# Optimization experiments

Measured on AMD Instinct MI355X. Metric: run time of the kernel, lower is better.

The kernel has to match this reference:

```python
import jax, jax.numpy as jnp
import numpy as np

N = 50000; E = 800000; G = 64; IN_DIM = 16; HID = 128; VOCAB = 10000; OUT = 768
# (prev_dim, heads, channels_per_head, concat) per GAT layer
LAYERS = [(128, 4, 128, True), (512, 4, 128, True), (512, 1, 128, False)]

def setup_inputs():
    keys = iter(jax.random.split(jax.random.key(0), 80))
    def nrm(shape, s=0.05):
        return jax.random.normal(next(keys), shape, jnp.float32) * s
    inp = {}
    inp["x"] = jax.random.normal(next(keys), (N, IN_DIM), jnp.float32)
    inp["node_ids"] = jax.random.randint(next(keys), (N,), 0, VOCAB)
    inp["edge_index"] = jax.random.randint(next(keys), (2, E), 0, N)
    inp["batch"] = jnp.sort(jax.random.randint(next(keys), (N,), 0, G))
    inp["emb"] = nrm((VOCAB, HID))
    inp["in_W"] = nrm((IN_DIM, HID)); inp["in_b"] = nrm((HID,))
    for i, (p, h, c, cat) in enumerate(LAYERS):
        od = h * c if cat else c
        inp[f"l{i}_lin_W"] = nrm((p, h * c))
        inp[f"l{i}_att_src"] = nrm((h, c))
        inp[f"l{i}_att_dst"] = nrm((h, c))
        inp[f"l{i}_bias"] = nrm((od,))
        inp[f"l{i}_bn_g"] = jnp.ones((od,), jnp.float32)
        inp[f"l{i}_bn_b"] = jnp.zeros((od,), jnp.float32)
        inp[f"l{i}_bn_m"] = nrm((od,))
        inp[f"l{i}_bn_v"] = jax.random.uniform(next(keys), (od,), jnp.float32, 0.5, 1.5)
        inp[f"l{i}_res_W"] = nrm((p, od)); inp[f"l{i}_res_b"] = nrm((od,))
    inp["out_W"] = nrm((2 * 128, OUT)); inp["out_b"] = nrm((OUT,))
    inp["ln_g"] = jnp.ones((OUT,), jnp.float32); inp["ln_b"] = jnp.zeros((OUT,), jnp.float32)
    return inp

def _gat(x, W, a_s, a_d, b, src, dst, h, c, cat):
    # PyG GATConv (eval): lin -> per-edge leaky_relu attention -> segment softmax over dst -> scatter-sum
    n = x.shape[0]
    xl = (x @ W).reshape(n, h, c)                       # [N,H,C]
    e = (xl * a_s).sum(-1)[src] + (xl * a_d).sum(-1)[dst]  # [E,H]
    e = jnp.where(e > 0, e, 0.2 * e)                    # leaky_relu, slope 0.2
    m = jax.ops.segment_max(e, dst, num_segments=n)
    ex = jnp.exp(e - m[dst])
    alpha = ex / jax.ops.segment_sum(ex, dst, num_segments=n)[dst]
    out = jax.ops.segment_sum(xl[src] * alpha[:, :, None], dst, num_segments=n)  # [N,H,C]
    out = out.reshape(n, h * c) if cat else out.mean(axis=1)
    return out + b

def _forward(x, node_ids, edge_index, batch, emb, in_W, in_b, layer_ps, out_W, out_b, ln_g, ln_b):
    n = x.shape[0]
    loop = jnp.arange(n)
    src = jnp.concatenate([edge_index[0], loop])        # GATConv adds self-loops
    dst = jnp.concatenate([edge_index[1], loop])
    h = x @ in_W + in_b + emb[node_ids]
    for (lin_W, a_s, a_d, bias, bn_g, bn_b, bn_m, bn_v, res_W, res_b), (p, nh, c, cat) in zip(layer_ps, LAYERS):
        y = _gat(h, lin_W, a_s, a_d, bias, src, dst, nh, c, cat)
        y = (y - bn_m) / jnp.sqrt(bn_v + 1e-5) * bn_g + bn_b   # BatchNorm1d eval
        y = jax.nn.relu(y)
        h = (h @ res_W + res_b) + y
    cnt = jax.ops.segment_sum(jnp.ones((n,), h.dtype), batch, num_segments=G)
    mean_pool = jax.ops.segment_sum(h, batch, num_segments=G) / jnp.maximum(cnt, 1.0)[:, None]
    max_pool = jax.ops.segment_max(h, batch, num_segments=G)
    max_pool = jnp.where(cnt[:, None] > 0, max_pool, 0.0)
    g = jnp.concatenate([mean_pool, max_pool], axis=-1)  # [G, 256]
    z = jax.nn.relu(g @ out_W + out_b)
    mu = z.mean(-1, keepdims=True)
    var = ((z - mu) ** 2).mean(-1, keepdims=True)
    return (z - mu) / jnp.sqrt(var + 1e-5) * ln_g + ln_b

def reference(x, node_ids, edge_index, batch, emb, in_W, in_b, l0_lin_W, l0_att_src, l0_att_dst, l0_bias, l0_bn_g, l0_bn_b, l0_bn_m, l0_bn_v, l0_res_W, l0_res_b, l1_lin_W, l1_att_src, l1_att_dst, l1_bias, l1_bn_g, l1_bn_b, l1_bn_m, l1_bn_v, l1_res_W, l1_res_b, l2_lin_W, l2_att_src, l2_att_dst, l2_bias, l2_bn_g, l2_bn_b, l2_bn_m, l2_bn_v, l2_res_W, l2_res_b, out_W, out_b, ln_g, ln_b):
    layer_ps = [
        (l0_lin_W, l0_att_src, l0_att_dst, l0_bias, l0_bn_g, l0_bn_b, l0_bn_m, l0_bn_v, l0_res_W, l0_res_b),
        (l1_lin_W, l1_att_src, l1_att_dst, l1_bias, l1_bn_g, l1_bn_b, l1_bn_m, l1_bn_v, l1_res_W, l1_res_b),
        (l2_lin_W, l2_att_src, l2_att_dst, l2_bias, l2_bn_g, l2_bn_b, l2_bn_m, l2_bn_v, l2_res_W, l2_res_b),
    ]
    return _forward(x, node_ids, edge_index, batch, emb, in_W, in_b, layer_ps, out_W, out_b, ln_g, ln_b)
```

## Files before the change

kernel.cpp:

```cpp
#include <hip/hip_runtime.h>

constexpr int N = 50000;
constexpr int G = 64;
constexpr int HID = 128;
constexpr int OUT = 768;
constexpr int MPAD = 50048;

typedef unsigned short u16;
typedef short s16x8 __attribute__((ext_vector_type(8)));
typedef float f32x4 __attribute__((ext_vector_type(4)));

__device__ inline float b2f(u16 b) { return __uint_as_float(((unsigned)b) << 16); }
__device__ inline u16 f2b(float f) {
    unsigned u = __float_as_uint(f);
    u += 0x7fff + ((u >> 16) & 1);
    return (u16)(u >> 16);
}

__device__ inline void gload16(const void* g, void* l) {
    __builtin_amdgcn_global_load_lds((const __attribute__((address_space(1))) void*)g,
                                     (__attribute__((address_space(3))) void*)l, 16, 0, 0);
}

__global__ void prep_k(const float* __restrict__ x, const int* __restrict__ ids,
                       const float* __restrict__ emb, const float* __restrict__ inW,
                       const float* __restrict__ inb, u16* __restrict__ h,
                       const int* __restrict__ ei, int* __restrict__ cnt, int E, int ET, int nbCnt,
                       const float* __restrict__ lin0, const float* __restrict__ res0, u16* __restrict__ w0,
                       const float* __restrict__ lin1, const float* __restrict__ res1, u16* __restrict__ w1,
                       const float* __restrict__ lin2, const float* __restrict__ res2, u16* __restrict__ w2) {
    int b = blockIdx.x, t = threadIdx.x;
    if (b < 25000) {
        int idx = b * 256 + t;
        int i = idx >> 7, j = idx & 127;
        float s = inb[j] + emb[(size_t)ids[i] * HID + j];
        const float* xr = x + (size_t)i * 16;
#pragma unroll
        for (int k = 0; k < 16; ++k) s += xr[k] * inW[k * HID + j];
        h[idx] = f2b(s);
    } else if (b < 25000 + nbCnt) {
        int e = (b - 25000) * 256 + t;
        if (e < ET) {
            int d = (e < E) ? ei[E + e] : (e - E);
            atomicAdd(&cnt[d], 1);
        }
    } else {
        int i = (b - 25000 - nbCnt) * 256 + t;
        const float* lin; const float* res; u16* dst; int p, od;
        if (i < 131072)      { lin = lin0; res = res0; dst = w0; p = 128; od = 512; }
        else if (i < 655360) { lin = lin1; res = res1; dst = w1; p = 512; od = 512; i -= 131072; }
        else if (i < 786432) { lin = lin2; res = res2; dst = w2; p = 512; od = 128; i -= 655360; }
        else return;
        int o = i / p, k = i - o * p;
        float v = (o < od) ? lin[(size_t)k * od + o] : res[(size_t)k * od + (o - od)];
        dst[i] = f2b(v);
    }
}

template<int LAYER, int H>
__global__ __launch_bounds__(256) void gemm2_k(const u16* __restrict__ A, const u16* __restrict__ Bt,
                                               const float* __restrict__ res_b,
                                               const float* __restrict__ a_s, const float* __restrict__ a_d,
                                               u16* __restrict__ xl, u16* __restrict__ rr,
                                               float* __restrict__ ssrc, float* __restrict__ sdst,
                                               int M, int od, int K) {
    __shared__ __align__(16) u16 lds[2][2][4096];
    int tid = threadIdx.x;
    int nbx = od >> 6;
    int nwg = gridDim.x;
    int qq = nwg >> 3, r8 = nwg & 7;
    int xcd = blockIdx.x & 7, ii = blockIdx.x >> 3;
    int swz = (xcd < r8 ? xcd * (qq + 1) : r8 * (qq + 1) + (xcd - r8) * qq) + ii;
    int bx = swz % nbx, by = swz / nbx;
    int row0 = by << 7, col0 = bx << 7;
    int wave = tid >> 6, lane = tid & 63;
    int wm = (wave & 1) << 6, wn = (wave >> 1) << 6;
    int lr = lane & 15, q = lane >> 4, lk8 = q << 3;

    const u16* ga = A + (size_t)(row0 + (tid >> 2)) * K + ((tid & 3) << 3);
    const u16* gb = Bt + (size_t)(col0 + (tid >> 2)) * K + ((tid & 3) << 3);

    f32x4 acc[4][4];
#pragma unroll
    for (int mf = 0; mf < 4; ++mf)
#pragma unroll
        for (int nf = 0; nf < 4; ++nf) acc[mf][nf] = {0.f, 0.f, 0.f, 0.f};

    auto stage = [&](int buf, int k0) {
        char* la = (char*)&lds[buf][0][0] + (wave << 10);
        char* lb = (char*)&lds[buf][1][0] + (wave << 10);
        gload16(ga + k0, la);
        gload16(ga + k0 + (size_t)64 * K, la + 4096);
        gload16(gb + k0, lb);
        gload16(gb + k0 + (size_t)64 * K, lb + 4096);
    };

    int nt = K >> 5;
    stage(0, 0);
    __syncthreads();
    int buf = 0;
    for (int t = 0; t < nt; ++t) {
        if (t + 1 < nt) stage(buf ^ 1, (t + 1) << 5);
        const u16* La = (const u16*)lds[buf][0];
        const u16* Lb = (const u16*)lds[buf][1];
        s16x8 af[4], bfr[4];
#pragma unroll
        for (int mf = 0; mf < 4; ++mf) af[mf] = *(const s16x8*)(La + (wm + mf * 16 + lr) * 32 + lk8);
#pragma unroll
        for (int nf = 0; nf < 4; ++nf) bfr[nf] = *(const s16x8*)(Lb + (wn + nf * 16 + lr) * 32 + lk8);
#pragma unroll
        for (int mf = 0; mf < 4; ++mf)
#pragma unroll
            for (int nf = 0; nf < 4; ++nf)
                acc[mf][nf] = __builtin_amdgcn_mfma_f32_16x16x32_bf16(bfr[nf], af[mf], acc[mf][nf], 0, 0, 0);
        __syncthreads();
        buf ^= 1;
    }

    bool isRes = (col0 >= od);
#pragma unroll
    for (int mf = 0; mf < 4; ++mf) {
        int row = row0 + wm + mf * 16 + lr;
        if (row < M) {
            if (isRes) {
#pragma unroll
                for (int nf = 0; nf < 4; ++nf) {
                    int c = (col0 - od) + wn + nf * 16 + (q << 2);
                    float4 bv = *(const float4*)(res_b + c);
                    unsigned lo = (unsigned)f2b(acc[mf][nf][0] + bv.x) | ((unsigned)f2b(acc[mf][nf][1] + bv.y) << 16);
                    unsigned hi = (unsigned)f2b(acc[mf][nf][2] + bv.z) | ((unsigned)f2b(acc[mf][nf][3] + bv.w) << 16);
                    uint2 pk; pk.x = lo; pk.y = hi;
                    *(uint2*)(rr + (size_t)row * od + c) = pk;
                }
            } else {
#pragma unroll
                for (int nf = 0; nf < 4; ++nf) {
                    int c = col0 + wn + nf * 16 + (q << 2);
                    unsigned lo = (unsigned)f2b(acc[mf][nf][0]) | ((unsigned)f2b(acc[mf][nf][1]) << 16);
                    unsigned hi = (unsigned)f2b(acc[mf][nf][2]) | ((unsigned)f2b(acc[mf][nf][3]) << 16);
                    uint2 pk; pk.x = lo; pk.y = hi;
                    *(uint2*)(xl + (size_t)row * od + c) = pk;
                }
            }
        }
    }
    if (!isRes) {
        int hh = (H == 4) ? (col0 >> 7) : 0;
        const float* asb = a_s + hh * 128 + wn + (q << 2);
        const float* adb = a_d + hh * 128 + wn + (q << 2);
        float4 as4[4], ad4[4];
#pragma unroll
        for (int nf = 0; nf < 4; ++nf) {
            as4[nf] = *(const float4*)(asb + nf * 16);
            ad4[nf] = *(const float4*)(adb + nf * 16);
        }
        float* sred = (float*)&lds[0][0][0];
#pragma unroll
        for (int mf = 0; mf < 4; ++mf) {
            float vs = 0.f, vd = 0.f;
#pragma unroll
            for (int nf = 0; nf < 4; ++nf) {
                vs += acc[mf][nf][0] * as4[nf].x + acc[mf][nf][1] * as4[nf].y
                    + acc[mf][nf][2] * as4[nf].z + acc[mf][nf][3] * as4[nf].w;
                vd += acc[mf][nf][0] * ad4[nf].x + acc[mf][nf][1] * ad4[nf].y
                    + acc[mf][nf][2] * ad4[nf].z + acc[mf][nf][3] * ad4[nf].w;
            }
            vs += __shfl_xor(vs, 16); vs += __shfl_xor(vs, 32);
            vd += __shfl_xor(vd, 16); vd += __shfl_xor(vd, 32);
            if (q == 0) {
                int rl = wm + mf * 16 + lr;
                sred[(wn >> 6) * 256 + rl * 2 + 0] = vs;
                sred[(wn >> 6) * 256 + rl * 2 + 1] = vd;
            }
        }
        __syncthreads();
        int rl = tid >> 1, which = tid & 1;
        int grow = row0 + rl;
        if (grow < M) {
            float v = sred[rl * 2 + which] + sred[256 + rl * 2 + which];
            if (which == 0) ssrc[grow * H + hh] = v;
            else            sdst[grow * H + hh] = v;
        }
    }
}

__global__ void bsum_k(const int* __restrict__ cnt, int* __restrict__ bsum) {
    __shared__ int sd[256];
    int t = threadIdx.x, i = blockIdx.x * 256 + t;
    sd[t] = (i < N) ? cnt[i] : 0;
    __syncthreads();
    for (int off = 128; off; off >>= 1) { if (t < off) sd[t] += sd[t + off]; __syncthreads(); }
    if (t == 0) bsum[blockIdx.x] = sd[0];
}

__global__ void scan2_k(const int* __restrict__ bsum, int* __restrict__ boff, int nb,
                        const int* __restrict__ batch, int* __restrict__ cntg) {
    if (blockIdx.x == 0) {
        __shared__ int sd[256];
        int t = threadIdx.x;
        int v = (t < nb) ? bsum[t] : 0;
        sd[t] = v;
        __syncthreads();
        for (int off = 1; off < 256; off <<= 1) {
            int tmp = (t >= off) ? sd[t - off] : 0;
            __syncthreads();
            sd[t] += tmp;
            __syncthreads();
        }
        if (t < nb) boff[t] = sd[t] - v;
    } else {
        int g = threadIdx.x;
        if (g >= G) return;
        int lo = 0, hi = N;
        while (lo < hi) { int mid = (lo + hi) >> 1; if (batch[mid] < g) lo = mid + 1; else hi = mid; }
        int lb0 = lo;
        lo = 0; hi = N;
        while (lo < hi) { int mid = (lo + hi) >> 1; if (batch[mid] < g + 1) lo = mid + 1; else hi = mid; }
        cntg[g] = lo - lb0;
    }
}

__global__ void iscan_k(const int* __restrict__ cnt, const int* __restrict__ boff,
                        int* __restrict__ indptr, int* __restrict__ fill) {
    __shared__ int sd[256];
    int b = blockIdx.x, t = threadIdx.x, i = b * 256 + t;
    int v = (i < N) ? cnt[i] : 0;
    sd[t] = v;
    __syncthreads();
    for (int off = 1; off < 256; off <<= 1) {
        int tmp = (t >= off) ? sd[t - off] : 0;
        __syncthreads();
        sd[t] += tmp;
        __syncthreads();
    }
    if (i < N) {
        int incl = boff[b] + sd[t];
        indptr[i + 1] = incl;
        fill[i] = incl - v;
    }
    if (i == 0) indptr[0] = 0;
}

__global__ void scatter_k(const int* __restrict__ ei, int* __restrict__ fill, int* __restrict__ out, int E, int ET) {
    int e = blockIdx.x * 256 + threadIdx.x;
    if (e >= ET) return;
    int s, d;
    if (e < E) { s = ei[e]; d = ei[E + e]; } else { s = d = e - E; }
    int pos = atomicAdd(&fill[d], 1);
    out[pos] = s;
}

template<int H, int OD>
__global__ __launch_bounds__(256) void agg_k(const u16* __restrict__ xl, const float* __restrict__ ssrc,
                                             const float* __restrict__ sdst, const int* __restrict__ indptr,
                                             const int* __restrict__ srcs, const float* __restrict__ bias,
                                             const float* __restrict__ bng, const float* __restrict__ bnb,
                                             const float* __restrict__ bnm, const float* __restrict__ bnv,
                                             u16* __restrict__ rr) {
    int w = (blockIdx.x * 256 + threadIdx.x) >> 6;
    int lane = threadIdx.x & 63;
    if (w >= N) return;
    int beg = indptr[w], deg = indptr[w + 1] - beg;
    constexpr int GRP = (H == 4) ? 16 : 64;
    int h = (H == 4) ? (lane >> 4) : 0;
    float sdl = sdst[w * H + h];
    float lmax = -3.4e38f, lsum = 0.f;
    int sub = lane & (GRP - 1);
    for (int e = sub; e < deg; e += GRP) {
        int s = srcs[beg + e];
        float v = ssrc[s * H + h] + sdl;
        v = v > 0.f ? v : 0.2f * v;
        lmax = fmaxf(lmax, v);
    }
#pragma unroll
    for (int o = GRP >> 1; o; o >>= 1) lmax = fmaxf(lmax, __shfl_xor(lmax, o));
    for (int e = sub; e < deg; e += GRP) {
        int s = srcs[beg + e];
        float v = ssrc[s * H + h] + sdl;
        v = v > 0.f ? v : 0.2f * v;
        lsum += __expf(v - lmax);
    }
#pragma unroll
    for (int o = GRP >> 1; o; o >>= 1) lsum += __shfl_xor(lsum, o);
    float inv = 1.0f / lsum;

    constexpr int EPL = OD / 64;
    float acc[EPL];
#pragma unroll
    for (int j = 0; j < EPL; ++j) acc[j] = 0.f;
    int e = 0;
    for (; e + 2 <= deg; e += 2) {
        int s0 = srcs[beg + e];
        int s1 = srcs[beg + e + 1];
        float v0 = ssrc[s0 * H + h] + sdl;
        float v1 = ssrc[s1 * H + h] + sdl;
        v0 = v0 > 0.f ? v0 : 0.2f * v0;
        v1 = v1 > 0.f ? v1 : 0.2f * v1;
        float wg0 = __expf(v0 - lmax) * inv;
        float wg1 = __expf(v1 - lmax) * inv;
        if constexpr (EPL == 8) {
            s16x8 xv0 = *(const s16x8*)(xl + (size_t)s0 * OD + lane * 8);
            s16x8 xv1 = *(const s16x8*)(xl + (size_t)s1 * OD + lane * 8);
#pragma unroll
            for (int j = 0; j < 8; ++j) acc[j] += b2f((u16)xv0[j]) * wg0;
#pragma unroll
            for (int j = 0; j < 8; ++j) acc[j] += b2f((u16)xv1[j]) * wg1;
        } else {
            unsigned xv0 = *(const unsigned*)(xl + (size_t)s0 * OD + lane * 2);
            unsigned xv1 = *(const unsigned*)(xl + (size_t)s1 * OD + lane * 2);
            acc[0] += b2f((u16)(xv0 & 0xffff)) * wg0;
            acc[1] += b2f((u16)(xv0 >> 16)) * wg0;
            acc[0] += b2f((u16)(xv1 & 0xffff)) * wg1;
            acc[1] += b2f((u16)(xv1 >> 16)) * wg1;
        }
    }
    for (; e < deg; ++e) {
        int s = srcs[beg + e];
        float v = ssrc[s * H + h] + sdl;
        v = v > 0.f ? v : 0.2f * v;
        float wg = __expf(v - lmax) * inv;
        if constexpr (EPL == 8) {
            s16x8 xv = *(const s16x8*)(xl + (size_t)s * OD + lane * 8);
#pragma unroll
            for (int j = 0; j < 8; ++j) acc[j] += b2f((u16)xv[j]) * wg;
        } else {
            unsigned xv = *(const unsigned*)(xl + (size_t)s * OD + lane * 2);
            acc[0] += b2f((u16)(xv & 0xffff)) * wg;
            acc[1] += b2f((u16)(xv >> 16)) * wg;
        }
    }
    if constexpr (EPL == 8) {
        s16x8 rv = *(const s16x8*)(rr + (size_t)w * OD + lane * 8);
        s16x8 ov;
#pragma unroll
        for (int j = 0; j < 8; ++j) {
            int c = lane * 8 + j;
            float v = acc[j] + bias[c] - bnm[c];
            v = v * rsqrtf(bnv[c] + 1e-5f) * bng[c] + bnb[c];
            ov[j] = (short)f2b(b2f((u16)rv[j]) + fmaxf(v, 0.f));
        }
        *(s16x8*)(rr + (size_t)w * OD + lane * 8) = ov;
    } else {
        unsigned rv = *(const unsigned*)(rr + (size_t)w * OD + lane * 2);
        unsigned o01 = 0;
#pragma unroll
        for (int j = 0; j < 2; ++j) {
            int c = lane * 2 + j;
            float v = acc[j] + bias[c] - bnm[c];
            v = v * rsqrtf(bnv[c] + 1e-5f) * bng[c] + bnb[c];
            float hv = b2f((u16)((rv >> (16 * j)) & 0xffff)) + fmaxf(v, 0.f);
            o01 |= ((unsigned)f2b(hv)) << (16 * j);
        }
        *(unsigned*)(rr + (size_t)w * OD + lane * 2) = o01;
    }
}

__device__ inline unsigned fkey(float f) {
    unsigned u = __float_as_uint(f);
    return (u & 0x80000000u) ? ~u : (u | 0x80000000u);
}

__global__ __launch_bounds__(128) void pool_k(const u16* __restrict__ h, const int* __restrict__ batch,
                                              float* __restrict__ psum, unsigned* __restrict__ pmax) {
    int c = threadIdx.x;
    int n0 = blockIdx.x * 64;
    if (n0 >= N) return;
    int nend = min(n0 + 64, N);
    int cur = batch[n0];
    float acc = 0.f, mx = -3.4e38f;
    for (int i = n0; i < nend; ++i) {
        int g = batch[i];
        if (g != cur) {
            atomicAdd(&psum[cur * 128 + c], acc);
            atomicMax(&pmax[cur * 128 + c], fkey(mx));
            acc = 0.f; mx = -3.4e38f; cur = g;
        }
        float v = b2f(h[(size_t)i * 128 + c]);
        acc += v;
        mx = fmaxf(mx, v);
    }
    atomicAdd(&psum[cur * 128 + c], acc);
    atomicMax(&pmax[cur * 128 + c], fkey(mx));
}

__global__ __launch_bounds__(768) void head_k(const float* __restrict__ psum, const unsigned* __restrict__ pmax,
                                              const int* __restrict__ cntg, const float* __restrict__ W,
                                              const float* __restrict__ b, const float* __restrict__ lng,
                                              const float* __restrict__ lnb, float* __restrict__ out) {
    __shared__ float gin[256];
    __shared__ float red[768];
    int g = blockIdx.x, t = threadIdx.x;
    int cg = cntg[g];
    if (t < 256) {
        float val;
        if (t < 128) {
            val = psum[g * 128 + t] / fmaxf((float)cg, 1.0f);
        } else {
            unsigned k = pmax[g * 128 + (t - 128)];
            if (cg > 0 && k != 0u) {
                unsigned u = (k & 0x80000000u) ? (k ^ 0x80000000u) : ~k;
                val = __uint_as_float(u);
            } else val = 0.0f;
        }
        gin[t] = val;
    }
    __syncthreads();
    float s = b[t];
    for (int k = 0; k < 256; ++k) s += gin[k] * W[(size_t)k * OUT + t];
    float z = fmaxf(s, 0.f);
    red[t] = z;
    __syncthreads();
    if (t < 256) red[t] = red[t] + red[t + 256] + red[t + 512];
    __syncthreads();
    for (int off = 128; off; off >>= 1) { if (t < off) red[t] += red[t + off]; __syncthreads(); }
    float mu = red[0] / 768.0f;
    __syncthreads();
    float d = z - mu;
    red[t] = d * d;
    __syncthreads();
    if (t < 256) red[t] = red[t] + red[t + 256] + red[t + 512];
    __syncthreads();
    for (int off = 128; off; off >>= 1) { if (t < off) red[t] += red[t + off]; __syncthreads(); }
    float inv = rsqrtf(red[0] / 768.0f + 1e-5f);
    out[(size_t)g * OUT + t] = d * inv * lng[t] + lnb[t];
}

extern "C" void kernel_launch(void* const* d_in, const int* in_sizes, int n_in,
                              void* d_out, int out_size, void* d_ws, size_t ws_size,
                              hipStream_t stream) {
    const float* x = (const float*)d_in[0];
    const int* node_ids = (const int*)d_in[1];
    const int* ei = (const int*)d_in[2];
    const int* batch = (const int*)d_in[3];
    const float* emb = (const float*)d_in[4];
    const float* in_W = (const float*)d_in[5];
    const float* in_b = (const float*)d_in[6];
    const float* L[3][10];
    for (int l = 0; l < 3; ++l)
        for (int q = 0; q < 10; ++q) L[l][q] = (const float*)d_in[7 + l * 10 + q];
    const float* out_W = (const float*)d_in[37];
    const float* out_b = (const float*)d_in[38];
    const float* ln_g = (const float*)d_in[39];
    const float* ln_b = (const float*)d_in[40];
    int E = in_sizes[2] / 2;
    int ET = E + N;
    const int NBLK = (N + 255) / 256;

    char* ws = (char*)d_ws;
    size_t off = 0;
    auto alloc = [&](size_t bytes) -> void* {
        void* p = ws + off;
        off += (bytes + 255) & ~(size_t)255;
        return p;
    };
    const size_t NBH = (size_t)MPAD * 512 * sizeof(u16);
    u16* bufA = (u16*)alloc(NBH);
    u16* bufB = (u16*)alloc(NBH);
    u16* bufC = (u16*)alloc(NBH);
    const int lp[3] = {128, 512, 512};
    const int lod[3] = {512, 512, 128};
    u16* wcomb[3];
    for (int l = 0; l < 3; ++l) wcomb[l] = (u16*)alloc((size_t)2 * lod[l] * lp[l] * sizeof(u16));
    float* ssrc = (float*)alloc((size_t)N * 4 * sizeof(float));
    float* sdst = (float*)alloc((size_t)N * 4 * sizeof(float));
    int* cnt = (int*)alloc((size_t)N * sizeof(int));
    int* indptr = (int*)alloc((size_t)(N + 1) * sizeof(int));
    int* fill = (int*)alloc((size_t)N * sizeof(int));
    int* ssorted = (int*)alloc((size_t)ET * sizeof(int));
    int* bsum = (int*)alloc(256 * sizeof(int));
    int* boff = (int*)alloc(256 * sizeof(int));
    float* psum = (float*)alloc(G * 128 * sizeof(float));
    unsigned* pmax = (unsigned*)alloc(G * 128 * sizeof(unsigned));
    int* cntg = (int*)alloc(G * sizeof(int));

    if (off > ws_size) return;

    hipMemsetAsync(cnt, 0, (size_t)N * sizeof(int), stream);
    hipMemsetAsync(psum, 0, G * 128 * sizeof(float), stream);
    hipMemsetAsync(pmax, 0, G * 128 * sizeof(unsigned), stream);

    int nbCnt = (ET + 255) / 256;
    prep_k<<<25000 + nbCnt + 3072, 256, 0, stream>>>(x, node_ids, emb, in_W, in_b, bufA,
                                                     ei, cnt, E, ET, nbCnt,
                                                     L[0][0], L[0][8], wcomb[0],
                                                     L[1][0], L[1][8], wcomb[1],
                                                     L[2][0], L[2][8], wcomb[2]);
    bsum_k<<<NBLK, 256, 0, stream>>>(cnt, bsum);
    scan2_k<<<2, 256, 0, stream>>>(bsum, boff, NBLK, batch, cntg);
    iscan_k<<<NBLK, 256, 0, stream>>>(cnt, boff, indptr, fill);
    scatter_k<<<(ET + 255) / 256, 256, 0, stream>>>(ei, fill, ssorted, E, ET);

    u16* h = bufA;
    u16* xb = bufB;
    u16* rb = bufC;
    const int nby = MPAD >> 7;
    for (int l = 0; l < 3; ++l) {
        int p = lp[l], od = lod[l];
        int nbx = od >> 6;
        int grid = nbx * nby;
        if (l == 0)
            gemm2_k<0, 4><<<grid, 256, 0, stream>>>(h, wcomb[l], L[l][9], L[l][1], L[l][2],
                                                    xb, rb, ssrc, sdst, N, od, p);
        else if (l == 1)
            gemm2_k<1, 4><<<grid, 256, 0, stream>>>(h, wcomb[l], L[l][9], L[l][1], L[l][2],
                                                    xb, rb, ssrc, sdst, N, od, p);
        else
            gemm2_k<2, 1><<<grid, 256, 0, stream>>>(h, wcomb[l], L[l][9], L[l][1], L[l][2],
                                                    xb, rb, ssrc, sdst, N, od, p);
        int sblocks = ((size_t)N * 64 + 255) / 256;
        if (l < 2)
            agg_k<4, 512><<<sblocks, 256, 0, stream>>>(xb, ssrc, sdst, indptr, ssorted,
                                                       L[l][3], L[l][4], L[l][5], L[l][6], L[l][7], rb);
        else
            agg_k<1, 128><<<sblocks, 256, 0, stream>>>(xb, ssrc, sdst, indptr, ssorted,
                                                       L[l][3], L[l][4], L[l][5], L[l][6], L[l][7], rb);
        u16* t2 = h; h = rb; rb = xb; xb = t2;
    }

    pool_k<<<(N + 63) / 64, 128, 0, stream>>>(h, batch, psum, pmax);
    head_k<<<G, 768, 0, stream>>>(psum, pmax, cntg, out_W, out_b, ln_g, ln_b, (float*)d_out);
}
```

Baseline: 820.3 us.

## Make GEMM blocks loop over multiple row tiles with cross-tile prefetch

The fused lin/residual GEMM now has each workgroup process up to TPB consecutive 128-row tiles for a fixed column block. It prefetches the next tile's first K-slice while running the epilogue of the current one, and the reduction scratch moves to its own LDS array. Layers 0 and 1 use four tiles per block, which cuts the grid size and launch overhead and hides the pipeline prologue behind the epilogue. The cost is fewer workgroups, so occupancy and load balance across CUs may drop.

```diff
diff --git a/kernel.cpp b/kernel.cpp
--- a/kernel.cpp
+++ b/kernel.cpp
@@ -57,7 +57,7 @@
     }
 }
 
-template<int LAYER, int H>
+template<int LAYER, int H, int TPB>
 __global__ __launch_bounds__(256) void gemm2_k(const u16* __restrict__ A, const u16* __restrict__ Bt,
                                                const float* __restrict__ res_b,
                                                const float* __restrict__ a_s, const float* __restrict__ a_d,
@@ -65,122 +65,131 @@
                                                float* __restrict__ ssrc, float* __restrict__ sdst,
                                                int M, int od, int K) {
     __shared__ __align__(16) u16 lds[2][2][4096];
+    __shared__ float sred[2][128][2];
     int tid = threadIdx.x;
     int nbx = od >> 6;
     int nwg = gridDim.x;
     int qq = nwg >> 3, r8 = nwg & 7;
     int xcd = blockIdx.x & 7, ii = blockIdx.x >> 3;
     int swz = (xcd < r8 ? xcd * (qq + 1) : r8 * (qq + 1) + (xcd - r8) * qq) + ii;
-    int bx = swz % nbx, by = swz / nbx;
-    int row0 = by << 7, col0 = bx << 7;
+    int bx = swz % nbx, chunk = swz / nbx;
+    int col0 = bx << 7;
+    int totTiles = (M + 127) >> 7;
+    int by0 = chunk * TPB;
+    if (by0 >= totTiles) return;
+    int ntiles = totTiles - by0; if (ntiles > TPB) ntiles = TPB;
     int wave = tid >> 6, lane = tid & 63;
     int wm = (wave & 1) << 6, wn = (wave >> 1) << 6;
     int lr = lane & 15, q = lane >> 4, lk8 = q << 3;
-
-    const u16* ga = A + (size_t)(row0 + (tid >> 2)) * K + ((tid & 3) << 3);
+    bool isRes = (col0 >= od);
+    int nt = K >> 5;
+
+    int aoff = (tid >> 2) * K + ((tid & 3) << 3);
     const u16* gb = Bt + (size_t)(col0 + (tid >> 2)) * K + ((tid & 3) << 3);
 
-    f32x4 acc[4][4];
-#pragma unroll
-    for (int mf = 0; mf < 4; ++mf)
-#pragma unroll
-        for (int nf = 0; nf < 4; ++nf) acc[mf][nf] = {0.f, 0.f, 0.f, 0.f};
-
-    auto stage = [&](int buf, int k0) {
+    auto stage = [&](int buf, int k0, int row0) {
         char* la = (char*)&lds[buf][0][0] + (wave << 10);
         char* lb = (char*)&lds[buf][1][0] + (wave << 10);
+        const u16* ga = A + (size_t)row0 * K + aoff;
         gload16(ga + k0, la);
         gload16(ga + k0 + (size_t)64 * K, la + 4096);
         gload16(gb + k0, lb);
         gload16(gb + k0 + (size_t)64 * K, lb + 4096);
     };
 
-    int nt = K >> 5;
-    stage(0, 0);
-    __syncthreads();
     int buf = 0;
-    for (int t = 0; t < nt; ++t) {
-        if (t + 1 < nt) stage(buf ^ 1, (t + 1) << 5);
-        const u16* La = (const u16*)lds[buf][0];
-        const u16* Lb = (const u16*)lds[buf][1];
-        s16x8 af[4], bfr[4];
-#pragma unroll
-        for (int mf = 0; mf < 4; ++mf) af[mf] = *(const s16x8*)(La + (wm + mf * 16 + lr) * 32 + lk8);
-#pragma unroll
-        for (int nf = 0; nf < 4; ++nf) bfr[nf] = *(const s16x8*)(Lb + (wn + nf * 16 + lr) * 32 + lk8);
+    stage(0, 0, by0 << 7);
+    for (int ti = 0; ti < ntiles; ++ti) {
+        int row0 = (by0 + ti) << 7;
+        __syncthreads();
+        f32x4 acc[4][4];
 #pragma unroll
         for (int mf = 0; mf < 4; ++mf)
 #pragma unroll
-            for (int nf = 0; nf < 4; ++nf)
-                acc[mf][nf] = __builtin_amdgcn_mfma_f32_16x16x32_bf16(bfr[nf], af[mf], acc[mf][nf], 0, 0, 0);
-        __syncthreads();
-        buf ^= 1;
-    }
-
-    bool isRes = (col0 >= od);
-#pragma unroll
-    for (int mf = 0; mf < 4; ++mf) {
-        int row = row0 + wm + mf * 16 + lr;
-        if (row < M) {
-            if (isRes) {
-#pragma unroll
-                for (int nf = 0; nf < 4; ++nf) {
-                    int c = (col0 - od) + wn + nf * 16 + (q << 2);
-                    float4 bv = *(const float4*)(res_b + c);
-                    unsigned lo = (unsigned)f2b(acc[mf][nf][0] + bv.x) | ((unsigned)f2b(acc[mf][nf][1] + bv.y) << 16);
-                    unsigned hi = (unsigned)f2b(acc[mf][nf][2] + bv.z) | ((unsigned)f2b(acc[mf][nf][3] + bv.w) << 16);
-                    uint2 pk; pk.x = lo; pk.y = hi;
-                    *(uint2*)(rr + (size_t)row * od + c) = pk;
-                }
-            } else {
-#pragma unroll
-                for (int nf = 0; nf < 4; ++nf) {
-                    int c = col0 + wn + nf * 16 + (q << 2);
-                    unsigned lo = (unsigned)f2b(acc[mf][nf][0]) | ((unsigned)f2b(acc[mf][nf][1]) << 16);
-                    unsigned hi = (unsigned)f2b(acc[mf][nf][2]) | ((unsigned)f2b(acc[mf][nf][3]) << 16);
-                    uint2 pk; pk.x = lo; pk.y = hi;
-                    *(uint2*)(xl + (size_t)row * od + c) = pk;
+            for (int nf = 0; nf < 4; ++nf) acc[mf][nf] = {0.f, 0.f, 0.f, 0.f};
+
+        for (int t = 0; t < nt; ++t) {
+            if (t + 1 < nt) stage(buf ^ 1, (t + 1) << 5, row0);
+            const u16* La = (const u16*)lds[buf][0];
+            const u16* Lb = (const u16*)lds[buf][1];
+            s16x8 af[4], bfr[4];
+#pragma unroll
+            for (int mf = 0; mf < 4; ++mf) af[mf] = *(const s16x8*)(La + (wm + mf * 16 + lr) * 32 + lk8);
+#pragma unroll
+            for (int nf = 0; nf < 4; ++nf) bfr[nf] = *(const s16x8*)(Lb + (wn + nf * 16 + lr) * 32 + lk8);
+#pragma unroll
+            for (int mf = 0; mf < 4; ++mf)
+#pragma unroll
+                for (int nf = 0; nf < 4; ++nf)
+                    acc[mf][nf] = __builtin_amdgcn_mfma_f32_16x16x32_bf16(bfr[nf], af[mf], acc[mf][nf], 0, 0, 0);
+            if (t + 1 < nt) { __syncthreads(); buf ^= 1; }
+        }
+        if (ti + 1 < ntiles) stage(buf ^ 1, 0, (by0 + ti + 1) << 7);
+
+#pragma unroll
+        for (int mf = 0; mf < 4; ++mf) {
+            int row = row0 + wm + mf * 16 + lr;
+            if (row < M) {
+                if (isRes) {
+#pragma unroll
+                    for (int nf = 0; nf < 4; ++nf) {
+                        int c = (col0 - od) + wn + nf * 16 + (q << 2);
+                        float4 bv = *(const float4*)(res_b + c);
+                        unsigned lo = (unsigned)f2b(acc[mf][nf][0] + bv.x) | ((unsigned)f2b(acc[mf][nf][1] + bv.y) << 16);
+                        unsigned hi = (unsigned)f2b(acc[mf][nf][2] + bv.z) | ((unsigned)f2b(acc[mf][nf][3] + bv.w) << 16);
+                        uint2 pk; pk.x = lo; pk.y = hi;
+                        *(uint2*)(rr + (size_t)row * od + c) = pk;
+                    }
+                } else {
+#pragma unroll
+                    for (int nf = 0; nf < 4; ++nf) {
+                        int c = col0 + wn + nf * 16 + (q << 2);
+                        unsigned lo = (unsigned)f2b(acc[mf][nf][0]) | ((unsigned)f2b(acc[mf][nf][1]) << 16);
+                        unsigned hi = (unsigned)f2b(acc[mf][nf][2]) | ((unsigned)f2b(acc[mf][nf][3]) << 16);
+                        uint2 pk; pk.x = lo; pk.y = hi;
+                        *(uint2*)(xl + (size_t)row * od + c) = pk;
+                    }
                 }
             }
         }
-    }
-    if (!isRes) {
-        int hh = (H == 4) ? (col0 >> 7) : 0;
-        const float* asb = a_s + hh * 128 + wn + (q << 2);
-        const float* adb = a_d + hh * 128 + wn + (q << 2);
-        float4 as4[4], ad4[4];
-#pragma unroll
-        for (int nf = 0; nf < 4; ++nf) {
-            as4[nf] = *(const float4*)(asb + nf * 16);
-            ad4[nf] = *(const float4*)(adb + nf * 16);
-        }
-        float* sred = (float*)&lds[0][0][0];
-#pragma unroll
-        for (int mf = 0; mf < 4; ++mf) {
-            float vs = 0.f, vd = 0.f;
+        if (!isRes) {
+            int hh = (H == 4) ? (col0 >> 7) : 0;
+            const float* asb = a_s + hh * 128 + wn + (q << 2);
+            const float* adb = a_d + hh * 128 + wn + (q << 2);
+            float4 as4[4], ad4[4];
 #pragma unroll
             for (int nf = 0; nf < 4; ++nf) {
-                vs += acc[mf][nf][0] * as4[nf].x + acc[mf][nf][1] * as4[nf].y
-                    + acc[mf][nf][2] * as4[nf].z + acc[mf][nf][3] * as4[nf].w;
-                vd += acc[mf][nf][0] * ad4[nf].x + acc[mf][nf][1] * ad4[nf].y
-                    + acc[mf][nf][2] * ad4[nf].z + acc[mf][nf][3] * ad4[nf].w;
+                as4[nf] = *(const float4*)(asb + nf * 16);
+                ad4[nf] = *(const float4*)(adb + nf * 16);
             }
-            vs += __shfl_xor(vs, 16); vs += __shfl_xor(vs, 32);
-            vd += __shfl_xor(vd, 16); vd += __shfl_xor(vd, 32);
-            if (q == 0) {
-                int rl = wm + mf * 16 + lr;
-                sred[(wn >> 6) * 256 + rl * 2 + 0] = vs;
-                sred[(wn >> 6) * 256 + rl * 2 + 1] = vd;
+#pragma unroll
+            for (int mf = 0; mf < 4; ++mf) {
+                float vs = 0.f, vd = 0.f;
+#pragma unroll
+                for (int nf = 0; nf < 4; ++nf) {
+                    vs += acc[mf][nf][0] * as4[nf].x + acc[mf][nf][1] * as4[nf].y
+                        + acc[mf][nf][2] * as4[nf].z + acc[mf][nf][3] * as4[nf].w;
+                    vd += acc[mf][nf][0] * ad4[nf].x + acc[mf][nf][1] * ad4[nf].y
+                        + acc[mf][nf][2] * ad4[nf].z + acc[mf][nf][3] * ad4[nf].w;
+                }
+                vs += __shfl_xor(vs, 16); vs += __shfl_xor(vs, 32);
+                vd += __shfl_xor(vd, 16); vd += __shfl_xor(vd, 32);
+                if (q == 0) {
+                    int rl = wm + mf * 16 + lr;
+                    sred[wn >> 6][rl][0] = vs;
+                    sred[wn >> 6][rl][1] = vd;
+                }
             }
-        }
-        __syncthreads();
-        int rl = tid >> 1, which = tid & 1;
-        int grow = row0 + rl;
-        if (grow < M) {
-            float v = sred[rl * 2 + which] + sred[256 + rl * 2 + which];
-            if (which == 0) ssrc[grow * H + hh] = v;
-            else            sdst[grow * H + hh] = v;
-        }
+            __syncthreads();
+            int rl = tid >> 1, which = tid & 1;
+            int grow = row0 + rl;
+            if (grow < M) {
+                float v = sred[0][rl][which] + sred[1][rl][which];
+                if (which == 0) ssrc[grow * H + hh] = v;
+                else            sdst[grow * H + hh] = v;
+            }
+        }
+        buf ^= 1;
     }
 }
 
@@ -493,20 +502,23 @@
     u16* h = bufA;
     u16* xb = bufB;
     u16* rb = bufC;
-    const int nby = MPAD >> 7;
+    const int totTiles = (N + 127) >> 7;
     for (int l = 0; l < 3; ++l) {
         int p = lp[l], od = lod[l];
         int nbx = od >> 6;
-        int grid = nbx * nby;
-        if (l == 0)
-            gemm2_k<0, 4><<<grid, 256, 0, stream>>>(h, wcomb[l], L[l][9], L[l][1], L[l][2],
-                                                    xb, rb, ssrc, sdst, N, od, p);
-        else if (l == 1)
-            gemm2_k<1, 4><<<grid, 256, 0, stream>>>(h, wcomb[l], L[l][9], L[l][1], L[l][2],
-                                                    xb, rb, ssrc, sdst, N, od, p);
-        else
-            gemm2_k<2, 1><<<grid, 256, 0, stream>>>(h, wcomb[l], L[l][9], L[l][1], L[l][2],
-                                                    xb, rb, ssrc, sdst, N, od, p);
+        if (l == 0) {
+            int grid = nbx * ((totTiles + 3) / 4);
+            gemm2_k<0, 4, 4><<<grid, 256, 0, stream>>>(h, wcomb[l], L[l][9], L[l][1], L[l][2],
+                                                       xb, rb, ssrc, sdst, N, od, p);
+        } else if (l == 1) {
+            int grid = nbx * ((totTiles + 3) / 4);
+            gemm2_k<1, 4, 4><<<grid, 256, 0, stream>>>(h, wcomb[l], L[l][9], L[l][1], L[l][2],
+                                                       xb, rb, ssrc, sdst, N, od, p);
+        } else {
+            int grid = nbx * totTiles;
+            gemm2_k<2, 1, 1><<<grid, 256, 0, stream>>>(h, wcomb[l], L[l][9], L[l][1], L[l][2],
+                                                       xb, rb, ssrc, sdst, N, od, p);
+        }
         int sblocks = ((size_t)N * 64 + 255) / 256;
         if (l < 2)
             agg_k<4, 512><<<sblocks, 256, 0, stream>>>(xb, ssrc, sdst, indptr, ssorted,
```

After: 955.2 us. 16.5% more time.
